# Performance work log

Hardware: AMD Instinct MI355X
Metric: run time of the kernel (lower is better)

## Reference

```python
import jax, jax.numpy as jnp
import numpy as np

V, E, H, B, S = 32000, 1024, 1024, 64, 128


def setup_inputs() -> dict:
    key = jax.random.key(0)
    ks = jax.random.split(key, 16)
    s = 0.02
    return {
        "input_seq": jax.random.randint(ks[0], (B, 1), 0, V),
        "hidden": jax.random.normal(ks[1], (1, B, H), jnp.float32),
        "cell": jax.random.normal(ks[2], (1, B, H), jnp.float32),
        "encoder_outputs": jax.random.normal(ks[3], (B, S, H), jnp.float32),
        "emb": jax.random.normal(ks[4], (V, E), jnp.float32) * s,
        "Wa_w": jax.random.normal(ks[5], (H, H), jnp.float32) * s,
        "Wa_b": jnp.zeros((H,), jnp.float32),
        "Ua_w": jax.random.normal(ks[6], (H, H), jnp.float32) * s,
        "Ua_b": jnp.zeros((H,), jnp.float32),
        "Va_w": jax.random.normal(ks[7], (1, H), jnp.float32) * s,
        "Va_b": jnp.zeros((1,), jnp.float32),
        "W_ih": jax.random.normal(ks[8], (4 * H, E + H), jnp.float32) * s,
        "W_hh": jax.random.normal(ks[9], (4 * H, H), jnp.float32) * s,
        "b_ih": jnp.zeros((4 * H,), jnp.float32),
        "b_hh": jnp.zeros((4 * H,), jnp.float32),
        "out_w": jax.random.normal(ks[10], (V, H), jnp.float32) * s,
        "out_b": jnp.zeros((V,), jnp.float32),
    }


def reference(input_seq, hidden, cell, encoder_outputs, emb, Wa_w, Wa_b, Ua_w, Ua_b,
              Va_w, Va_b, W_ih, W_hh, b_ih, b_hh, out_w, out_b):
    # embedding lookup (dropout p=0 -> identity): [B,1,E]
    embedded = emb[input_seq]
    # query = last layer hidden: [B,1,H]
    query = hidden[-1][:, None, :]
    # Bahdanau additive attention
    q_proj = query @ Wa_w.T + Wa_b                       # [B,1,H]
    k_proj = encoder_outputs @ Ua_w.T + Ua_b             # [B,S,H]
    scores = jnp.tanh(q_proj + k_proj) @ Va_w.T + Va_b   # [B,S,1]
    scores = scores[..., 0][:, None, :]                  # [B,1,S]
    weights = jax.nn.softmax(scores, axis=-1)            # [B,1,S]
    context = jnp.einsum('bqs,bsh->bqh', weights, encoder_outputs)  # [B,1,H]
    # LSTM single step on concat(embedded, context)
    x = jnp.concatenate([embedded, context], axis=2)[:, 0, :]  # [B,E+H]
    h0, c0 = hidden[0], cell[0]
    gates = x @ W_ih.T + b_ih + h0 @ W_hh.T + b_hh       # [B,4H]
    i, f, g, o = jnp.split(gates, 4, axis=-1)
    c1 = jax.nn.sigmoid(f) * c0 + jax.nn.sigmoid(i) * jnp.tanh(g)
    h1 = jax.nn.sigmoid(o) * jnp.tanh(c1)
    output = h1[:, None, :]                              # [B,1,H]
    logits = output @ out_w.T + out_b                    # [B,1,V]
    return logits, h1[None], c1[None], weights
```

## Files before the change

kernel.cpp:

```cpp
#include <hip/hip_runtime.h>
#include <hip/hip_bf16.h>

using short8 = __attribute__((ext_vector_type(8))) short;
using f32x4  = __attribute__((ext_vector_type(4))) float;

__device__ inline unsigned pk2(float lo, float hi) {
    __hip_bfloat162 h = __float22bfloat162_rn(float2{lo, hi});
    return *reinterpret_cast<unsigned*>(&h);
}
__device__ inline short8 cvt8(float4 a, float4 b) {
    union { unsigned u[4]; short8 s; } r;
    r.u[0] = pk2(a.x, a.y); r.u[1] = pk2(a.z, a.w);
    r.u[2] = pk2(b.x, b.y); r.u[3] = pk2(b.z, b.w);
    return r.s;
}
__device__ inline float ftanh(float x) {
    float e = __expf(2.f * x);
    return 1.f - 2.f / (e + 1.f);
}

__device__ inline void gload16(const void* g, void* lds) {
    __builtin_amdgcn_global_load_lds(
        (const __attribute__((address_space(1))) unsigned int*)g,
        (__attribute__((address_space(3))) unsigned int*)lds, 16, 0, 0);
}

__global__ void k_zero(float4* __restrict__ p, int n) {
    for (int i = blockIdx.x * blockDim.x + threadIdx.x; i < n;
         i += gridDim.x * blockDim.x) {
        float4 z = {0.f, 0.f, 0.f, 0.f};
        p[i] = z;
    }
}

__global__ void k_cvt_swz(const float* __restrict__ src, short* __restrict__ dst,
                          int granules) {
    int i = blockIdx.x * blockDim.x + threadIdx.x;
    if (i >= granules) return;
    int row = i >> 7, gi = i & 127;
    int seg = gi >> 3, g = gi & 7;
    const float* p = src + ((size_t)row << 10) + (seg << 6) + ((g ^ (row & 7)) << 3);
    float4 v0 = *(const float4*)p;
    float4 v1 = *(const float4*)(p + 4);
    *(short8*)&dst[(size_t)i << 3] = cvt8(v0, v1);
}

__global__ __launch_bounds__(256) void k_attn2(
    const short* __restrict__ Abf, const short* __restrict__ Bbf,
    const float* __restrict__ Uab, const float* __restrict__ Wab,
    const float* __restrict__ qp, const float* __restrict__ Va,
    float* __restrict__ scores) {
    __shared__ short As[128 * 64];
    __shared__ short Bs[128 * 64];
    const int t = threadIdx.x;
    const int l = t & 63, w = t >> 6;
    const int wm = w >> 1, wn = w & 1;
    const int lr = l & 15, lg = l >> 4;
    const int n0 = blockIdx.x * 128;
    const int r0 = blockIdx.y * 128;
    const int lrow8 = l >> 3, lgr = l & 7;

    f32x4 acc[4][4];
#pragma unroll
    for (int i = 0; i < 4; ++i)
#pragma unroll
        for (int j = 0; j < 4; ++j) { f32x4 z = {0.f, 0.f, 0.f, 0.f}; acc[i][j] = z; }

    for (int seg = 0; seg < 16; ++seg) {
#pragma unroll
        for (int i = 0; i < 4; ++i) {
            int arow = w * 32 + i * 8;
            gload16(Abf + (size_t)(r0 + arow + lrow8) * 1024 + seg * 64 + lgr * 8,
                    (void*)&As[arow * 64]);
            gload16(Bbf + (size_t)(n0 + arow + lrow8) * 1024 + seg * 64 + lgr * 8,
                    (void*)&Bs[arow * 64]);
        }
        __syncthreads();
#pragma unroll
        for (int kh = 0; kh < 2; ++kh) {
            short8 a[4], b[4];
#pragma unroll
            for (int i = 0; i < 4; ++i) {
                int ra = wm * 64 + i * 16 + lr;
                a[i] = *(const short8*)&As[ra * 64 + (((kh * 4 + lg) ^ (ra & 7)) << 3)];
                int rb = wn * 64 + i * 16 + lr;
                b[i] = *(const short8*)&Bs[rb * 64 + (((kh * 4 + lg) ^ (rb & 7)) << 3)];
            }
#pragma unroll
            for (int i = 0; i < 4; ++i)
#pragma unroll
                for (int j = 0; j < 4; ++j)
                    acc[i][j] = __builtin_amdgcn_mfma_f32_16x16x32_bf16(a[i], b[j], acc[i][j], 0, 0, 0);
        }
        __syncthreads();
    }

    const float* qpb = qp + blockIdx.y * 1024;
    float va[4], ub[4];
#pragma unroll
    for (int j = 0; j < 4; ++j) {
        int h = n0 + wn * 64 + j * 16 + lr;
        va[j] = Va[h];
        ub[j] = Uab[h] + Wab[h];
    }
#pragma unroll
    for (int i = 0; i < 4; ++i)
#pragma unroll
        for (int r = 0; r < 4; ++r) {
            int row = r0 + wm * 64 + i * 16 + lg * 4 + r;
            float s = 0.f;
#pragma unroll
            for (int j = 0; j < 4; ++j) {
                int h = n0 + wn * 64 + j * 16 + lr;
                s += va[j] * ftanh(acc[i][j][r] + qpb[h] + ub[j]);
            }
            s += __shfl_xor(s, 1);
            s += __shfl_xor(s, 2);
            s += __shfl_xor(s, 4);
            s += __shfl_xor(s, 8);
            if (lr == 0) atomicAdd(scores + row, s);
        }
}

__global__ __launch_bounds__(512, 2) void k_attn(
    const float* __restrict__ enc, const float* __restrict__ Ua,
    const float* __restrict__ Uab, const float* __restrict__ Wab,
    const float* __restrict__ qp, const float* __restrict__ Va,
    float* __restrict__ scores) {
    __shared__ short As[256 * 64];
    __shared__ short Bs[128 * 64];
    const int t = threadIdx.x;
    const int l = t & 63, w = t >> 6;
    const int wm = w >> 1, wn = w & 1;
    const int lr = l & 15, lg = l >> 4;
    const int n0 = blockIdx.x * 128;
    const int r0 = blockIdx.y * 256;

    f32x4 acc[4][4];
#pragma unroll
    for (int i = 0; i < 4; ++i)
#pragma unroll
        for (int j = 0; j < 4; ++j) { f32x4 z = {0.f, 0.f, 0.f, 0.f}; acc[i][j] = z; }

    auto stage = [&](int kt) {
#pragma unroll
        for (int i = 0; i < 4; ++i) {
            int s = t + 512 * i, row = s >> 3, ch = s & 7;
            const float* p = enc + (size_t)(r0 + row) * 1024 + kt + ch * 8;
            *(short8*)&As[row * 64 + ((ch ^ (row & 7)) << 3)] =
                cvt8(*(const float4*)p, *(const float4*)(p + 4));
        }
#pragma unroll
        for (int i = 0; i < 2; ++i) {
            int s = t + 512 * i, row = s >> 3, ch = s & 7;
            const float* p = Ua + (size_t)(n0 + row) * 1024 + kt + ch * 8;
            *(short8*)&Bs[row * 64 + ((ch ^ (row & 7)) << 3)] =
                cvt8(*(const float4*)p, *(const float4*)(p + 4));
        }
    };
    auto compute = [&]() {
#pragma unroll
        for (int kh = 0; kh < 2; ++kh) {
            short8 a[4], b[4];
#pragma unroll
            for (int i = 0; i < 4; ++i) {
                int row = wm * 64 + i * 16 + lr;
                a[i] = *(short8*)&As[row * 64 + ((((kh << 2) | lg) ^ (row & 7)) << 3)];
            }
#pragma unroll
            for (int j = 0; j < 4; ++j) {
                int row = wn * 64 + j * 16 + lr;
                b[j] = *(short8*)&Bs[row * 64 + ((((kh << 2) | lg) ^ (row & 7)) << 3)];
            }
#pragma unroll
            for (int i = 0; i < 4; ++i)
#pragma unroll
                for (int j = 0; j < 4; ++j)
                    acc[i][j] = __builtin_amdgcn_mfma_f32_16x16x32_bf16(a[i], b[j], acc[i][j], 0, 0, 0);
        }
    };

    for (int kt = 0; kt < 1024; kt += 64) {
        stage(kt);
        __syncthreads();
        compute();
        __syncthreads();
    }

    float va[4], ub[4];
#pragma unroll
    for (int j = 0; j < 4; ++j) {
        int h = n0 + wn * 64 + j * 16 + lr;
        va[j] = Va[h];
        ub[j] = Uab[h] + Wab[h];
    }
#pragma unroll
    for (int i = 0; i < 4; ++i)
#pragma unroll
        for (int r = 0; r < 4; ++r) {
            int row = r0 + wm * 64 + i * 16 + lg * 4 + r;
            const float* qpb = qp + (row >> 7) * 1024;
            float s = 0.f;
#pragma unroll
            for (int j = 0; j < 4; ++j) {
                int h = n0 + wn * 64 + j * 16 + lr;
                s += va[j] * ftanh(acc[i][j][r] + qpb[h] + ub[j]);
            }
            s += __shfl_xor(s, 1);
            s += __shfl_xor(s, 2);
            s += __shfl_xor(s, 4);
            s += __shfl_xor(s, 8);
            if (lr == 0) atomicAdd(scores + row, s);
        }
}

__global__ __launch_bounds__(256) void k_sgemm(
    const float* __restrict__ A, int lda,
    const float* __restrict__ B0, int ldb0,
    const float* __restrict__ B1, int ldb1, int kyB1,
    float* __restrict__ C, int ldc, int Kblk) {
    __shared__ short As[64 * 64];
    __shared__ short Bs[64 * 64];
    const int t = threadIdx.x;
    const int l = t & 63, w = t >> 6;
    const int wm = w >> 1, wn = w & 1;
    const int lr = l & 15, lg = l >> 4;
    const int n0 = blockIdx.x * 64;
    const int ky = blockIdx.y;

    const float* Ab = A + (size_t)ky * Kblk;
    const float* Bb;
    int ldb;
    if (ky < kyB1) { Bb = B0 + (size_t)ky * Kblk; ldb = ldb0; }
    else           { Bb = B1 + (size_t)(ky - kyB1) * Kblk; ldb = ldb1; }

    f32x4 acc[2][2];
#pragma unroll
    for (int i = 0; i < 2; ++i)
#pragma unroll
        for (int j = 0; j < 2; ++j) { f32x4 z = {0.f, 0.f, 0.f, 0.f}; acc[i][j] = z; }

    for (int kt = 0; kt < Kblk; kt += 64) {
#pragma unroll
        for (int i = 0; i < 2; ++i) {
            int s = t + 256 * i, row = s >> 3, ch = s & 7;
            const float* p = Ab + (size_t)row * lda + kt + ch * 8;
            *(short8*)&As[row * 64 + ((ch ^ (row & 7)) << 3)] =
                cvt8(*(const float4*)p, *(const float4*)(p + 4));
            const float* q = Bb + (size_t)(n0 + row) * ldb + kt + ch * 8;
            *(short8*)&Bs[row * 64 + ((ch ^ (row & 7)) << 3)] =
                cvt8(*(const float4*)q, *(const float4*)(q + 4));
        }
        __syncthreads();
#pragma unroll
        for (int kh = 0; kh < 2; ++kh) {
            short8 a[2], b[2];
#pragma unroll
            for (int i = 0; i < 2; ++i) {
                int ra = wm * 32 + i * 16 + lr;
                a[i] = *(const short8*)&As[ra * 64 + (((kh * 4 + lg) ^ (ra & 7)) << 3)];
                int rb = wn * 32 + i * 16 + lr;
                b[i] = *(const short8*)&Bs[rb * 64 + (((kh * 4 + lg) ^ (rb & 7)) << 3)];
            }
#pragma unroll
            for (int i = 0; i < 2; ++i)
#pragma unroll
                for (int j = 0; j < 2; ++j)
                    acc[i][j] = __builtin_amdgcn_mfma_f32_16x16x32_bf16(a[i], b[j], acc[i][j], 0, 0, 0);
        }
        __syncthreads();
    }

#pragma unroll
    for (int i = 0; i < 2; ++i)
#pragma unroll
        for (int j = 0; j < 2; ++j)
#pragma unroll
            for (int r = 0; r < 4; ++r) {
                int R = wm * 32 + i * 16 + lg * 4 + r;
                int c = n0 + wn * 32 + j * 16 + lr;
                atomicAdd(&C[(size_t)R * ldc + c], acc[i][j][r]);
            }
}

__global__ void k_biasinit(const float* __restrict__ ob, float* __restrict__ logits) {
    int i = blockIdx.x * blockDim.x + threadIdx.x;
    if (i >= 512000) return;
    int c4 = i - (i / 8000) * 8000;
    ((float4*)logits)[i] = ((const float4*)ob)[c4];
}

__global__ void k_gather(const int* __restrict__ idx, const float* __restrict__ emb,
                         const float* __restrict__ h0, float* __restrict__ xcat) {
    int b = blockIdx.x;
    int row = idx[b];
    const float4* se = (const float4*)(emb + (size_t)row * 1024);
    const float4* sh = (const float4*)(h0 + (size_t)b * 1024);
    float4* d = (float4*)(xcat + (size_t)b * 3072);
    for (int i = threadIdx.x; i < 256; i += blockDim.x) {
        d[i] = se[i];
        d[512 + i] = sh[i];
    }
}

__global__ void k_softmax(const float* __restrict__ scores, float* __restrict__ wout) {
    int b = blockIdx.x;
    int s = threadIdx.x;
    __shared__ float buf[128];
    float v = scores[b * 128 + s];
    buf[s] = v;
    __syncthreads();
    for (int off = 64; off > 0; off >>= 1) {
        if (s < off) buf[s] = fmaxf(buf[s], buf[s + off]);
        __syncthreads();
    }
    float m = buf[0];
    __syncthreads();
    float e = expf(v - m);
    buf[s] = e;
    __syncthreads();
    for (int off = 64; off > 0; off >>= 1) {
        if (s < off) buf[s] += buf[s + off];
        __syncthreads();
    }
    float sum = buf[0];
    wout[b * 128 + s] = e / sum;
}

__global__ void k_context(const float* __restrict__ enc, const float* __restrict__ w,
                          float* __restrict__ xcat) {
    int b = blockIdx.y;
    int t = threadIdx.x;
    int h = blockIdx.x * 256 + t;
    __shared__ float wsb[128];
    if (t < 128) wsb[t] = w[b * 128 + t];
    __syncthreads();
    float acc = 0.f;
#pragma unroll 4
    for (int s = 0; s < 128; ++s)
        acc += wsb[s] * enc[((size_t)b * 128 + s) * 1024 + h];
    xcat[(size_t)b * 3072 + 1024 + h] = acc;
}

__global__ void k_lstm(const float* __restrict__ gates, const float* __restrict__ c0,
                       const float* __restrict__ b_ih, const float* __restrict__ b_hh,
                       float* __restrict__ h1, float* __restrict__ c1) {
    int idx = blockIdx.x * blockDim.x + threadIdx.x;
    int b = idx >> 10, h = idx & 1023;
    const float* g = gates + (size_t)b * 4096;
    float iv = g[h] + b_ih[h] + b_hh[h];
    float fv = g[1024 + h] + b_ih[1024 + h] + b_hh[1024 + h];
    float gv = g[2048 + h] + b_ih[2048 + h] + b_hh[2048 + h];
    float ov = g[3072 + h] + b_ih[3072 + h] + b_hh[3072 + h];
    float si = 1.f / (1.f + expf(-iv));
    float sf = 1.f / (1.f + expf(-fv));
    float so = 1.f / (1.f + expf(-ov));
    float tg = tanhf(gv);
    float cc = sf * c0[idx] + si * tg;
    float hh = so * tanhf(cc);
    c1[idx] = cc;
    h1[idx] = hh;
}

extern "C" void kernel_launch(void* const* d_in, const int* in_sizes, int n_in,
                              void* d_out, int out_size, void* d_ws, size_t ws_size,
                              hipStream_t stream) {
    const int* idx = (const int*)d_in[0];
    const float* hidden = (const float*)d_in[1];
    const float* cell = (const float*)d_in[2];
    const float* enc = (const float*)d_in[3];
    const float* emb = (const float*)d_in[4];
    const float* Wa_w = (const float*)d_in[5];
    const float* Wa_b = (const float*)d_in[6];
    const float* Ua_w = (const float*)d_in[7];
    const float* Ua_b = (const float*)d_in[8];
    const float* Va_w = (const float*)d_in[9];
    const float* W_ih = (const float*)d_in[11];
    const float* W_hh = (const float*)d_in[12];
    const float* b_ih = (const float*)d_in[13];
    const float* b_hh = (const float*)d_in[14];
    const float* out_w = (const float*)d_in[15];
    const float* out_b = (const float*)d_in[16];

    float* out = (float*)d_out;
    float* logits = out;
    float* h1 = out + 2048000;
    float* c1 = out + 2048000 + 65536;
    float* wts = out + 2048000 + 65536 + 65536;

    float* ws = (float*)d_ws;
    float* qp = ws;
    float* scores = ws + 65536;
    float* gates = ws + 73728;
    float* xcat = ws + 335872;
    short* enc_bf = (short*)(ws + 532480);
    short* ua_bf  = enc_bf + 8192 * 1024;
    const size_t ws_need = 532480u * 4u + (8192u * 1024u + 1024u * 1024u) * 2u;
    const bool big_ws = ws_size >= ws_need;

    k_zero<<<192, 256, 0, stream>>>((float4*)ws, 83968);

    if (big_ws) {
        k_cvt_swz<<<4096, 256, 0, stream>>>(enc, enc_bf, 8192 * 128);
        k_cvt_swz<<<512, 256, 0, stream>>>(Ua_w, ua_bf, 1024 * 128);
    }
    k_gather<<<64, 256, 0, stream>>>(idx, emb, hidden, xcat);
    k_sgemm<<<dim3(16, 8), 256, 0, stream>>>(hidden, 1024, Wa_w, 1024,
                                             nullptr, 0, 99, qp, 1024, 128);
    if (big_ws)
        k_attn2<<<dim3(8, 64), 256, 0, stream>>>(enc_bf, ua_bf, Ua_b, Wa_b, qp, Va_w, scores);
    else
        k_attn<<<dim3(8, 32), 512, 0, stream>>>(enc, Ua_w, Ua_b, Wa_b, qp, Va_w, scores);
    k_softmax<<<64, 128, 0, stream>>>(scores, wts);
    k_context<<<dim3(4, 64), 256, 0, stream>>>(enc, wts, xcat);
    k_sgemm<<<dim3(64, 12), 256, 0, stream>>>(xcat, 3072, W_ih, 2048,
                                              W_hh, 1024, 8, gates, 4096, 256);
    k_lstm<<<256, 256, 0, stream>>>(gates, cell, b_ih, b_hh, h1, c1);
    k_biasinit<<<2000, 256, 0, stream>>>(out_b, logits);
    k_sgemm<<<dim3(500, 4), 256, 0, stream>>>(h1, 1024, out_w, 1024,
                                              nullptr, 0, 99, logits, 32000, 256);
}
```

Before: 142.9 us.

## Fuse init kernels, merge bf16 conversions, fuse softmax with context, enlarge attention tiles

Zeroing, bias init of logits and the embedding/hidden gather are merged into one k_init launch, and the two bf16 conversion launches become one. Softmax and the context weighted sum are fused into k_smctx. The attention GEMM now uses 512-thread blocks with 256-row tiles loaded via global_load_lds from the combined buffer. The small-workspace fallback is removed, so the code now assumes the workspace always fits the bf16 copies. The aim is fewer launches and better A-tile reuse, at the cost of only 64 blocks doing the context reduction.

Result: faster. 135.0 us (-5.6%).

```diff
diff --git a/kernel.cpp b/kernel.cpp
--- a/kernel.cpp
+++ b/kernel.cpp
@@ -18,112 +18,52 @@
     float e = __expf(2.f * x);
     return 1.f - 2.f / (e + 1.f);
 }
-
 __device__ inline void gload16(const void* g, void* lds) {
     __builtin_amdgcn_global_load_lds(
         (const __attribute__((address_space(1))) unsigned int*)g,
         (__attribute__((address_space(3))) unsigned int*)lds, 16, 0, 0);
 }
 
-__global__ void k_zero(float4* __restrict__ p, int n) {
-    for (int i = blockIdx.x * blockDim.x + threadIdx.x; i < n;
-         i += gridDim.x * blockDim.x) {
+__global__ void k_init(const float* __restrict__ ob, float* __restrict__ logits,
+                       const int* __restrict__ idx, const float* __restrict__ emb,
+                       const float* __restrict__ h0, float* __restrict__ xcat,
+                       float4* __restrict__ wsz) {
+    int i = blockIdx.x * blockDim.x + threadIdx.x;
+    if (i < 83968) {
         float4 z = {0.f, 0.f, 0.f, 0.f};
-        p[i] = z;
-    }
-}
-
-__global__ void k_cvt_swz(const float* __restrict__ src, short* __restrict__ dst,
-                          int granules) {
+        wsz[i] = z;
+    } else if (i < 595968) {
+        int j = i - 83968;
+        int c4 = j - (j / 8000) * 8000;
+        ((float4*)logits)[j] = ((const float4*)ob)[c4];
+    } else if (i < 645120) {
+        int j = i - 595968;
+        int b = j / 768, q = j - b * 768;
+        if (q < 256)
+            ((float4*)(xcat + (size_t)b * 3072))[q] =
+                ((const float4*)(emb + (size_t)idx[b] * 1024))[q];
+        else if (q >= 512)
+            ((float4*)(xcat + (size_t)b * 3072))[q] =
+                ((const float4*)(h0 + (size_t)b * 1024))[q - 512];
+    }
+}
+
+__global__ void k_cvt_swz(const float* __restrict__ enc, const float* __restrict__ Ua,
+                          short* __restrict__ dst) {
     int i = blockIdx.x * blockDim.x + threadIdx.x;
-    if (i >= granules) return;
+    if (i >= 9216 * 128) return;
     int row = i >> 7, gi = i & 127;
     int seg = gi >> 3, g = gi & 7;
-    const float* p = src + ((size_t)row << 10) + (seg << 6) + ((g ^ (row & 7)) << 3);
+    const float* src = (row < 8192) ? enc + ((size_t)row << 10)
+                                    : Ua + ((size_t)(row - 8192) << 10);
+    const float* p = src + (seg << 6) + ((g ^ (row & 7)) << 3);
     float4 v0 = *(const float4*)p;
     float4 v1 = *(const float4*)(p + 4);
     *(short8*)&dst[(size_t)i << 3] = cvt8(v0, v1);
 }
 
-__global__ __launch_bounds__(256) void k_attn2(
+__global__ __launch_bounds__(512) void k_attn2(
     const short* __restrict__ Abf, const short* __restrict__ Bbf,
-    const float* __restrict__ Uab, const float* __restrict__ Wab,
-    const float* __restrict__ qp, const float* __restrict__ Va,
-    float* __restrict__ scores) {
-    __shared__ short As[128 * 64];
-    __shared__ short Bs[128 * 64];
-    const int t = threadIdx.x;
-    const int l = t & 63, w = t >> 6;
-    const int wm = w >> 1, wn = w & 1;
-    const int lr = l & 15, lg = l >> 4;
-    const int n0 = blockIdx.x * 128;
-    const int r0 = blockIdx.y * 128;
-    const int lrow8 = l >> 3, lgr = l & 7;
-
-    f32x4 acc[4][4];
-#pragma unroll
-    for (int i = 0; i < 4; ++i)
-#pragma unroll
-        for (int j = 0; j < 4; ++j) { f32x4 z = {0.f, 0.f, 0.f, 0.f}; acc[i][j] = z; }
-
-    for (int seg = 0; seg < 16; ++seg) {
-#pragma unroll
-        for (int i = 0; i < 4; ++i) {
-            int arow = w * 32 + i * 8;
-            gload16(Abf + (size_t)(r0 + arow + lrow8) * 1024 + seg * 64 + lgr * 8,
-                    (void*)&As[arow * 64]);
-            gload16(Bbf + (size_t)(n0 + arow + lrow8) * 1024 + seg * 64 + lgr * 8,
-                    (void*)&Bs[arow * 64]);
-        }
-        __syncthreads();
-#pragma unroll
-        for (int kh = 0; kh < 2; ++kh) {
-            short8 a[4], b[4];
-#pragma unroll
-            for (int i = 0; i < 4; ++i) {
-                int ra = wm * 64 + i * 16 + lr;
-                a[i] = *(const short8*)&As[ra * 64 + (((kh * 4 + lg) ^ (ra & 7)) << 3)];
-                int rb = wn * 64 + i * 16 + lr;
-                b[i] = *(const short8*)&Bs[rb * 64 + (((kh * 4 + lg) ^ (rb & 7)) << 3)];
-            }
-#pragma unroll
-            for (int i = 0; i < 4; ++i)
-#pragma unroll
-                for (int j = 0; j < 4; ++j)
-                    acc[i][j] = __builtin_amdgcn_mfma_f32_16x16x32_bf16(a[i], b[j], acc[i][j], 0, 0, 0);
-        }
-        __syncthreads();
-    }
-
-    const float* qpb = qp + blockIdx.y * 1024;
-    float va[4], ub[4];
-#pragma unroll
-    for (int j = 0; j < 4; ++j) {
-        int h = n0 + wn * 64 + j * 16 + lr;
-        va[j] = Va[h];
-        ub[j] = Uab[h] + Wab[h];
-    }
-#pragma unroll
-    for (int i = 0; i < 4; ++i)
-#pragma unroll
-        for (int r = 0; r < 4; ++r) {
-            int row = r0 + wm * 64 + i * 16 + lg * 4 + r;
-            float s = 0.f;
-#pragma unroll
-            for (int j = 0; j < 4; ++j) {
-                int h = n0 + wn * 64 + j * 16 + lr;
-                s += va[j] * ftanh(acc[i][j][r] + qpb[h] + ub[j]);
-            }
-            s += __shfl_xor(s, 1);
-            s += __shfl_xor(s, 2);
-            s += __shfl_xor(s, 4);
-            s += __shfl_xor(s, 8);
-            if (lr == 0) atomicAdd(scores + row, s);
-        }
-}
-
-__global__ __launch_bounds__(512, 2) void k_attn(
-    const float* __restrict__ enc, const float* __restrict__ Ua,
     const float* __restrict__ Uab, const float* __restrict__ Wab,
     const float* __restrict__ qp, const float* __restrict__ Va,
     float* __restrict__ scores) {
@@ -142,35 +82,27 @@
 #pragma unroll
         for (int j = 0; j < 4; ++j) { f32x4 z = {0.f, 0.f, 0.f, 0.f}; acc[i][j] = z; }
 
-    auto stage = [&](int kt) {
+    for (int seg = 0; seg < 16; ++seg) {
 #pragma unroll
         for (int i = 0; i < 4; ++i) {
-            int s = t + 512 * i, row = s >> 3, ch = s & 7;
-            const float* p = enc + (size_t)(r0 + row) * 1024 + kt + ch * 8;
-            *(short8*)&As[row * 64 + ((ch ^ (row & 7)) << 3)] =
-                cvt8(*(const float4*)p, *(const float4*)(p + 4));
-        }
-#pragma unroll
-        for (int i = 0; i < 2; ++i) {
-            int s = t + 512 * i, row = s >> 3, ch = s & 7;
-            const float* p = Ua + (size_t)(n0 + row) * 1024 + kt + ch * 8;
-            *(short8*)&Bs[row * 64 + ((ch ^ (row & 7)) << 3)] =
-                cvt8(*(const float4*)p, *(const float4*)(p + 4));
-        }
-    };
-    auto compute = [&]() {
+            int base = i * 512 + w * 64;
+            int s = base + l;
+            gload16(Abf + (((size_t)r0 + (s >> 3)) << 10) + (seg << 6) + ((s & 7) << 3),
+                    (void*)&As[base * 8]);
+            if (i < 2)
+                gload16(Bbf + (((size_t)8192 + n0 + (s >> 3)) << 10) + (seg << 6) + ((s & 7) << 3),
+                        (void*)&Bs[base * 8]);
+        }
+        __syncthreads();
 #pragma unroll
         for (int kh = 0; kh < 2; ++kh) {
             short8 a[4], b[4];
 #pragma unroll
             for (int i = 0; i < 4; ++i) {
-                int row = wm * 64 + i * 16 + lr;
-                a[i] = *(short8*)&As[row * 64 + ((((kh << 2) | lg) ^ (row & 7)) << 3)];
-            }
-#pragma unroll
-            for (int j = 0; j < 4; ++j) {
-                int row = wn * 64 + j * 16 + lr;
-                b[j] = *(short8*)&Bs[row * 64 + ((((kh << 2) | lg) ^ (row & 7)) << 3)];
+                int ra = wm * 64 + i * 16 + lr;
+                a[i] = *(const short8*)&As[ra * 64 + (((kh * 4 + lg) ^ (ra & 7)) << 3)];
+                int rb = wn * 64 + i * 16 + lr;
+                b[i] = *(const short8*)&Bs[rb * 64 + (((kh * 4 + lg) ^ (rb & 7)) << 3)];
             }
 #pragma unroll
             for (int i = 0; i < 4; ++i)
@@ -178,12 +110,6 @@
                 for (int j = 0; j < 4; ++j)
                     acc[i][j] = __builtin_amdgcn_mfma_f32_16x16x32_bf16(a[i], b[j], acc[i][j], 0, 0, 0);
         }
-    };
-
-    for (int kt = 0; kt < 1024; kt += 64) {
-        stage(kt);
-        __syncthreads();
-        compute();
         __syncthreads();
     }
 
@@ -199,7 +125,7 @@
 #pragma unroll
         for (int r = 0; r < 4; ++r) {
             int row = r0 + wm * 64 + i * 16 + lg * 4 + r;
-            const float* qpb = qp + (row >> 7) * 1024;
+            const float* qpb = qp + (size_t)(row >> 7) * 1024;
             float s = 0.f;
 #pragma unroll
             for (int j = 0; j < 4; ++j) {
@@ -283,63 +209,56 @@
             }
 }
 
-__global__ void k_biasinit(const float* __restrict__ ob, float* __restrict__ logits) {
-    int i = blockIdx.x * blockDim.x + threadIdx.x;
-    if (i >= 512000) return;
-    int c4 = i - (i / 8000) * 8000;
-    ((float4*)logits)[i] = ((const float4*)ob)[c4];
-}
-
-__global__ void k_gather(const int* __restrict__ idx, const float* __restrict__ emb,
-                         const float* __restrict__ h0, float* __restrict__ xcat) {
+__global__ __launch_bounds__(256) void k_smctx(
+    const float* __restrict__ scores, const float* __restrict__ enc,
+    float* __restrict__ wout, float* __restrict__ xcat) {
     int b = blockIdx.x;
-    int row = idx[b];
-    const float4* se = (const float4*)(emb + (size_t)row * 1024);
-    const float4* sh = (const float4*)(h0 + (size_t)b * 1024);
-    float4* d = (float4*)(xcat + (size_t)b * 3072);
-    for (int i = threadIdx.x; i < 256; i += blockDim.x) {
-        d[i] = se[i];
-        d[512 + i] = sh[i];
-    }
-}
-
-__global__ void k_softmax(const float* __restrict__ scores, float* __restrict__ wout) {
-    int b = blockIdx.x;
-    int s = threadIdx.x;
+    int t = threadIdx.x;
     __shared__ float buf[128];
-    float v = scores[b * 128 + s];
-    buf[s] = v;
-    __syncthreads();
-    for (int off = 64; off > 0; off >>= 1) {
-        if (s < off) buf[s] = fmaxf(buf[s], buf[s + off]);
-        __syncthreads();
-    }
-    float m = buf[0];
-    __syncthreads();
-    float e = expf(v - m);
-    buf[s] = e;
-    __syncthreads();
-    for (int off = 64; off > 0; off >>= 1) {
-        if (s < off) buf[s] += buf[s + off];
-        __syncthreads();
-    }
-    float sum = buf[0];
-    wout[b * 128 + s] = e / sum;
-}
-
-__global__ void k_context(const float* __restrict__ enc, const float* __restrict__ w,
-                          float* __restrict__ xcat) {
-    int b = blockIdx.y;
-    int t = threadIdx.x;
-    int h = blockIdx.x * 256 + t;
     __shared__ float wsb[128];
-    if (t < 128) wsb[t] = w[b * 128 + t];
-    __syncthreads();
-    float acc = 0.f;
-#pragma unroll 4
-    for (int s = 0; s < 128; ++s)
-        acc += wsb[s] * enc[((size_t)b * 128 + s) * 1024 + h];
-    xcat[(size_t)b * 3072 + 1024 + h] = acc;
+    if (t < 128) buf[t] = scores[b * 128 + t];
+    __syncthreads();
+    if (t < 64) buf[t] = fmaxf(buf[t], buf[t + 64]);
+    __syncthreads();
+    if (t < 32) buf[t] = fmaxf(buf[t], buf[t + 32]);
+    __syncthreads();
+    float m;
+    {
+        float v = buf[t & 31];
+        for (int off = 16; off > 0; off >>= 1)
+            v = fmaxf(v, __shfl_xor(v, off, 32));
+        m = v;
+    }
+    __syncthreads();
+    if (t < 128) wsb[t] = __expf(scores[b * 128 + t] - m);
+    __syncthreads();
+    if (t < 64) buf[t] = wsb[t] + wsb[t + 64];
+    __syncthreads();
+    if (t < 32) buf[t] += buf[t + 32];
+    __syncthreads();
+    float sum;
+    {
+        float v = buf[t & 31];
+        for (int off = 16; off > 0; off >>= 1)
+            v += __shfl_xor(v, off, 32);
+        sum = v;
+    }
+    float inv = 1.f / sum;
+    __syncthreads();
+    if (t < 128) {
+        wsb[t] *= inv;
+        wout[b * 128 + t] = wsb[t];
+    }
+    __syncthreads();
+    float acc[4] = {0.f, 0.f, 0.f, 0.f};
+    for (int s = 0; s < 128; ++s) {
+        float wv = wsb[s];
+        const float* row = enc + ((size_t)b * 128 + s) * 1024;
+#pragma unroll
+        for (int j = 0; j < 4; ++j) acc[j] += wv * row[t + 256 * j];
+    }
+#pragma unroll
+    for (int j = 0; j < 4; ++j) xcat[(size_t)b * 3072 + 1024 + t + 256 * j] = acc[j];
 }
 
 __global__ void k_lstm(const float* __restrict__ gates, const float* __restrict__ c0,
@@ -393,30 +312,19 @@
     float* scores = ws + 65536;
     float* gates = ws + 73728;
     float* xcat = ws + 335872;
-    short* enc_bf = (short*)(ws + 532480);
-    short* ua_bf  = enc_bf + 8192 * 1024;
-    const size_t ws_need = 532480u * 4u + (8192u * 1024u + 1024u * 1024u) * 2u;
-    const bool big_ws = ws_size >= ws_need;
-
-    k_zero<<<192, 256, 0, stream>>>((float4*)ws, 83968);
-
-    if (big_ws) {
-        k_cvt_swz<<<4096, 256, 0, stream>>>(enc, enc_bf, 8192 * 128);
-        k_cvt_swz<<<512, 256, 0, stream>>>(Ua_w, ua_bf, 1024 * 128);
-    }
-    k_gather<<<64, 256, 0, stream>>>(idx, emb, hidden, xcat);
+    short* encua_bf = (short*)(ws + 532480);
+
+    k_init<<<2520, 256, 0, stream>>>(out_b, logits, idx, emb, hidden, xcat,
+                                     (float4*)ws);
+    k_cvt_swz<<<4608, 256, 0, stream>>>(enc, Ua_w, encua_bf);
     k_sgemm<<<dim3(16, 8), 256, 0, stream>>>(hidden, 1024, Wa_w, 1024,
                                              nullptr, 0, 99, qp, 1024, 128);
-    if (big_ws)
-        k_attn2<<<dim3(8, 64), 256, 0, stream>>>(enc_bf, ua_bf, Ua_b, Wa_b, qp, Va_w, scores);
-    else
-        k_attn<<<dim3(8, 32), 512, 0, stream>>>(enc, Ua_w, Ua_b, Wa_b, qp, Va_w, scores);
-    k_softmax<<<64, 128, 0, stream>>>(scores, wts);
-    k_context<<<dim3(4, 64), 256, 0, stream>>>(enc, wts, xcat);
+    k_attn2<<<dim3(8, 32), 512, 0, stream>>>(encua_bf, encua_bf, Ua_b, Wa_b,
+                                             qp, Va_w, scores);
+    k_smctx<<<64, 256, 0, stream>>>(scores, enc, wts, xcat);
     k_sgemm<<<dim3(64, 12), 256, 0, stream>>>(xcat, 3072, W_ih, 2048,
                                               W_hh, 1024, 8, gates, 4096, 256);
     k_lstm<<<256, 256, 0, stream>>>(gates, cell, b_ih, b_hh, h1, c1);
-    k_biasinit<<<2000, 256, 0, stream>>>(out_b, logits);
     k_sgemm<<<dim3(500, 4), 256, 0, stream>>>(h1, 1024, out_w, 1024,
                                               nullptr, 0, 99, logits, 32000, 256);
 }
```
